# Optimization experiments

Hardware: AMD Instinct MI355X
Metric: run time of the kernel (lower is better)

Reference implementation:

```python
import jax, jax.numpy as jnp
import numpy as np
import math

N, N_OBS, D, H, P = 500000, 200000, 32, 128, 4


def setup_inputs() -> dict:
    key = jax.random.key(0)
    ks = jax.random.split(key, 10)
    h = jax.random.normal(ks[0], (N, H), dtype=jnp.float32)
    p = jax.random.normal(ks[1], (N, 2 * D), dtype=jnp.float32)
    X_obs = jax.random.normal(ks[2], (N_OBS, D), dtype=jnp.float32)
    M_obs = (jax.random.uniform(ks[3], (N_OBS, D)) > 0.5).astype(jnp.float32)
    # unique sorted indices into [0, N) so the scatter-update is well defined
    i_obs = jnp.sort(jax.random.permutation(ks[4], N)[:N_OBS]).astype(jnp.int32)
    std = math.sqrt(2.0 / (4 + P))
    w_prep = std * jax.random.normal(ks[5], (D, 4, P), dtype=jnp.float32)
    bias_prep = 0.1 + jnp.zeros((D, P), dtype=jnp.float32)
    k = 1.0 / math.sqrt(H)
    W_ih = jax.random.uniform(ks[6], (3 * H, P * D), minval=-k, maxval=k, dtype=jnp.float32)
    W_hh = jax.random.uniform(ks[7], (3 * H, H), minval=-k, maxval=k, dtype=jnp.float32)
    b_ih = jax.random.uniform(ks[8], (3 * H,), minval=-k, maxval=k, dtype=jnp.float32)
    b_hh = jax.random.uniform(ks[9], (3 * H,), minval=-k, maxval=k, dtype=jnp.float32)
    return {"h": h, "p": p, "X_obs": X_obs, "M_obs": M_obs, "i_obs": i_obs,
            "w_prep": w_prep, "bias_prep": bias_prep,
            "W_ih": W_ih, "W_hh": W_hh, "b_ih": b_ih, "b_hh": b_hh}


def gru_cell(x, h, W_ih, W_hh, b_ih, b_hh):
    # torch.nn.GRUCell semantics; gate order r, z, n
    gi = x @ W_ih.T + b_ih            # [n, 3H]
    gh = h @ W_hh.T + b_hh            # [n, 3H]
    i_r, i_z, i_n = jnp.split(gi, 3, axis=1)
    h_r, h_z, h_n = jnp.split(gh, 3, axis=1)
    r = jax.nn.sigmoid(i_r + h_r)
    z = jax.nn.sigmoid(i_z + h_z)
    n = jnp.tanh(i_n + r * h_n)
    return (1.0 - z) * n + z * h


def reference(h, p, X_obs, M_obs, i_obs, w_prep, bias_prep, W_ih, W_hh, b_ih, b_hh):
    p_obs = p[i_obs]                                     # gather [n_obs, 2D]
    mean, logvar = jnp.split(p_obs, 2, axis=1)
    lv = jnp.clip(logvar, -10.0, 10.0)
    sigma = jnp.clip(jnp.exp(0.5 * lv), 1e-6, 1e6)
    error = jnp.clip((X_obs - mean) / sigma, -1e6, 1e6)
    log_lik_c = float(np.log(np.sqrt(2 * np.pi)))
    losses = 0.5 * ((error ** 2 + lv + 2.0 * log_lik_c) * M_obs)  # [n_obs, D]
    feats = jnp.stack([X_obs, mean, lv, error], axis=2)  # [n_obs, D, 4]
    gi = jnp.einsum('ndk,dkp->ndp', feats, w_prep) + bias_prep  # per-channel small matmul
    gi = jax.nn.relu(gi) * M_obs[..., None]              # mask broadcast over prep_hidden
    gru_in = gi.reshape(gi.shape[0], D * P)              # [n_obs, D*P], D-major like torch view
    h_obs = h[i_obs]
    h_new = gru_cell(gru_in, h_obs, W_ih, W_hh, b_ih, b_hh)
    h = h.at[i_obs].set(h_new)                           # scatter update
    return (h, losses)
```

## Files before the change

### kernel.cpp

```cpp
#include <hip/hip_runtime.h>


typedef __attribute__((ext_vector_type(8))) short bf16x8;
typedef __attribute__((ext_vector_type(4))) float f32x4;

__device__ inline unsigned short f2bf_rne(float x) {
    union { float f; unsigned int u; } v; v.f = x;
    unsigned int r = (v.u + 0x7fffu + ((v.u >> 16) & 1u)) >> 16;
    return (unsigned short)r;
}
__device__ inline unsigned short f2bf_tr(float x) {
    return (unsigned short)(__float_as_uint(x) >> 16);
}
__device__ inline float bf2f(unsigned short u) {
    return __uint_as_float(((unsigned int)u) << 16);
}
__device__ inline float fast_sigmoid(float x) {
    return __builtin_amdgcn_rcpf(1.f + __expf(-x));
}
__device__ inline float fast_tanh(float x) {
    const float a = fabsf(x);
    const float t = __expf(-2.f * a);
    const float r = (1.f - t) * __builtin_amdgcn_rcpf(1.f + t);
    return __builtin_copysignf(r, x);
}
__device__ inline void gl_lds16(const float* g, float* lds_base) {
    __builtin_amdgcn_global_load_lds(
        (const __attribute__((address_space(1))) void*)g,
        (__attribute__((address_space(3))) void*)lds_base, 16, 0, 0);
}

__global__ __launch_bounds__(256) void k_prepack(const float* __restrict__ W_ih,
                                                 const float* __restrict__ W_hh,
                                                 unsigned short* __restrict__ B) {
    const int i = blockIdx.x * 256 + threadIdx.x;
    const int w    = i / 12288;
    const int rem  = i - w * 12288;
    const int f    = rem >> 9;
    const int rem2 = rem & 511;
    const int l    = rem2 >> 3;
    const int j    = rem2 & 7;
    const int c    = w * 16 + (l & 15);
    const int ko   = (l >> 4) * 8 + j;
    float val;
    if (f < 8) {
        const int k = f * 32 + ko;
        val = (k < 128) ? W_ih[c * 128 + k] : W_hh[c * 128 + (k - 128)];
    } else if (f < 16) {
        const int k = (f - 8) * 32 + ko;
        val = (k < 128) ? W_ih[(128 + c) * 128 + k] : W_hh[(128 + c) * 128 + (k - 128)];
    } else if (f < 20) {
        const int k = (f - 16) * 32 + ko;
        val = W_ih[(256 + c) * 128 + k];
    } else {
        const int k = (f - 20 + 4) * 32 + ko;
        val = W_hh[(256 + c) * 128 + (k - 128)];
    }
    B[i] = f2bf_rne(val);
}

__global__ __launch_bounds__(256) void k_flag(const int* __restrict__ i_obs,
                                              unsigned char* __restrict__ flags, int n) {
    const int i = blockIdx.x * 256 + threadIdx.x;
    if (i < n) flags[i_obs[i]] = 1;
}

__global__ __launch_bounds__(256) void k_copy(const f32x4* __restrict__ src,
                                              f32x4* __restrict__ dst, long n4) {
    long i = (long)blockIdx.x * blockDim.x + threadIdx.x;
    long stride = (long)gridDim.x * blockDim.x;
    for (; i < n4; i += stride) dst[i] = src[i];
}

struct PrefRegs {
    float mean[4], lv[4], X[4], M[4];
    f32x4 hv[4];
    int idx[4];
};

__global__ __launch_bounds__(512) void k_pers(
    const float* __restrict__ h, const float* __restrict__ p,
    const float* __restrict__ X_obs, const float* __restrict__ M_obs,
    const int* __restrict__ i_obs,
    const float* __restrict__ w_prep, const float* __restrict__ bias_prep,
    const unsigned short* __restrict__ Bpk,
    const float* __restrict__ b_ih, const float* __restrict__ b_hh,
    float* __restrict__ out_h, float* __restrict__ out_losses,
    const unsigned char* __restrict__ flags,
    int NT, int chunk, int Nh, int do_copy)
{
    __shared__ unsigned short sA[4 * 8 * 64 * 8];
    __shared__ float hcopy[160 * 128];
    __shared__ int sIdx[64];

    const int tid  = threadIdx.x;
    const int d    = tid & 31;
    const int wid  = tid >> 6;
    const int lane = tid & 63;
    const int cw   = wid * 16 + (lane & 15);

    float wp[16], bp[4];
    #pragma unroll
    for (int t = 0; t < 16; ++t) wp[t] = w_prep[d * 16 + t];
    #pragma unroll
    for (int t = 0; t < 4; ++t) bp[t] = bias_prep[d * 4 + t];

    bf16x8 breg[24];
    {
        const bf16x8* bsrc = reinterpret_cast<const bf16x8*>(Bpk) + wid * 1536;
        #pragma unroll
        for (int f = 0; f < 24; ++f) breg[f] = bsrc[f * 64 + lane];
    }
    const float bR  = b_ih[cw]       + b_hh[cw];
    const float bZ  = b_ih[128 + cw] + b_hh[128 + cw];
    const float bIN = b_ih[256 + cw];
    const float bHN = b_hh[256 + cw];

    const int ksA  = d >> 3;
    const int l16  = ((d >> 1) & 3) * 16;
    const int j0   = (d & 1) * 4;
    const int ksE  = 4 + (cw >> 5);
    const int l16E = ((cw >> 3) & 3) * 16;
    const int jE   = cw & 7;

    const bf16x8* aptr = reinterpret_cast<const bf16x8*>(sA);

    PrefRegs R;

    auto G_load = [&](int t) {
        const int row0 = t * 64;
        #pragma unroll
        for (int ps = 0; ps < 4; ++ps) {
            const int r   = ps * 16 + (tid >> 5);
            const int idx = i_obs[row0 + r];
            R.idx[ps]  = idx;
            R.mean[ps] = p[(size_t)idx * 64 + d];
            R.lv[ps]   = p[(size_t)idx * 64 + 32 + d];
            R.X[ps]    = X_obs[(size_t)(row0 + r) * 32 + d];
            R.M[ps]    = M_obs[(size_t)(row0 + r) * 32 + d];
            R.hv[ps]   = *reinterpret_cast<const f32x4*>(h + (size_t)idx * 128 + d * 4);
        }
    };

    auto COPY_issue = [&](int t) {
        const long rlo = (long)t * chunk;
        const float* hs = h + rlo * 128;
        const int rbase = wid * 20;
        #pragma unroll
        for (int q = 0; q < 10; ++q) {
            const int row = rbase + q * 2;
            gl_lds16(hs + (size_t)row * 128 + lane * 4, &hcopy[row * 128]);
        }
    };

    auto COPY_store = [&](int t) {
        const long rlo = (long)t * chunk;
        f32x4* hd = reinterpret_cast<f32x4*>(out_h + rlo * 128);
        const unsigned char* fl = flags + rlo;
        const f32x4* hc = reinterpret_cast<const f32x4*>(hcopy);
        #pragma unroll
        for (int ii = 0; ii < 10; ++ii) {
            const int i5 = ii * 512 + tid;
            if (!fl[i5 >> 5]) __builtin_nontemporal_store(hc[i5], &hd[i5]);
        }
    };

    auto C_phase = [&](int t) {
        const int row0 = t * 64;
        #pragma unroll
        for (int ps = 0; ps < 4; ++ps) {
            const int r  = ps * 16 + (tid >> 5);
            const int mt = r >> 4;
            if (d == 0) sIdx[r] = R.idx[ps];
            const float lv      = fminf(fmaxf(R.lv[ps], -10.f), 10.f);
            const float inv_sig = __expf(-0.5f * lv);
            const float X = R.X[ps], Mv = R.M[ps], mean = R.mean[ps];
            const float err = fminf(fmaxf((X - mean) * inv_sig, -1e6f), 1e6f);
            out_losses[(size_t)(row0 + r) * 32 + d] =
                0.5f * ((err * err + lv + 1.8378770664093453f) * Mv);
            ushort4 u;
            float g0 = fmaf(X, wp[0], fmaf(mean, wp[4], fmaf(lv, wp[8],  fmaf(err, wp[12], bp[0]))));
            float g1 = fmaf(X, wp[1], fmaf(mean, wp[5], fmaf(lv, wp[9],  fmaf(err, wp[13], bp[1]))));
            float g2 = fmaf(X, wp[2], fmaf(mean, wp[6], fmaf(lv, wp[10], fmaf(err, wp[14], bp[2]))));
            float g3 = fmaf(X, wp[3], fmaf(mean, wp[7], fmaf(lv, wp[11], fmaf(err, wp[15], bp[3]))));
            u.x = f2bf_tr(fmaxf(g0, 0.f) * Mv);
            u.y = f2bf_tr(fmaxf(g1, 0.f) * Mv);
            u.z = f2bf_tr(fmaxf(g2, 0.f) * Mv);
            u.w = f2bf_tr(fmaxf(g3, 0.f) * Mv);
            *reinterpret_cast<ushort4*>(&sA[((mt * 8 + ksA) * 64 + (r & 15) + l16) * 8 + j0]) = u;
            const f32x4 v = R.hv[ps];
            ushort4 uh;
            uh.x = f2bf_tr(v.x); uh.y = f2bf_tr(v.y); uh.z = f2bf_tr(v.z); uh.w = f2bf_tr(v.w);
            *reinterpret_cast<ushort4*>(&sA[((mt * 8 + ksA + 4) * 64 + (r & 15) + l16) * 8 + j0]) = uh;
        }
    };

    auto M_phase = [&]() {
        #pragma unroll
        for (int mt = 0; mt < 4; ++mt) {
            f32x4 accR = {0.f, 0.f, 0.f, 0.f};
            f32x4 accZ = {0.f, 0.f, 0.f, 0.f};
            f32x4 accIN = {0.f, 0.f, 0.f, 0.f};
            f32x4 accHN = {0.f, 0.f, 0.f, 0.f};
            #pragma unroll
            for (int ks = 0; ks < 8; ++ks) {
                const bf16x8 af = aptr[(mt * 8 + ks) * 64 + lane];
                accR = __builtin_amdgcn_mfma_f32_16x16x32_bf16(af, breg[ks],     accR, 0, 0, 0);
                accZ = __builtin_amdgcn_mfma_f32_16x16x32_bf16(af, breg[8 + ks], accZ, 0, 0, 0);
                if (ks < 4) accIN = __builtin_amdgcn_mfma_f32_16x16x32_bf16(af, breg[16 + ks], accIN, 0, 0, 0);
                else        accHN = __builtin_amdgcn_mfma_f32_16x16x32_bf16(af, breg[16 + ks], accHN, 0, 0, 0);
            }
            const int r15b = (lane >> 4) * 4;
            #pragma unroll
            for (int reg = 0; reg < 4; ++reg) {
                const int r15 = r15b + reg;
                const int idx = sIdx[mt * 16 + r15];
                const float hp = bf2f(sA[((mt * 8 + ksE) * 64 + r15 + l16E) * 8 + jE]);
                const float xr  = accR[reg]  + bR;
                const float xz  = accZ[reg]  + bZ;
                const float xin = accIN[reg] + bIN;
                const float xhn = accHN[reg] + bHN;
                const float rg = fast_sigmoid(xr);
                const float zg = fast_sigmoid(xz);
                const float ng = fast_tanh(fmaf(rg, xhn, xin));
                out_h[(size_t)idx * 128 + cw] = fmaf(zg, hp - ng, ng);
            }
        }
    };

    int t = blockIdx.x;
    if (t >= NT) return;
    const int stride = gridDim.x;

    G_load(t);
    C_phase(t);
    __syncthreads();

    for (;;) {
        const int tn = t + stride;
        const bool has_next = (tn < NT);
        if (has_next) G_load(tn);
        if (do_copy) COPY_issue(t);
        M_phase();
        __syncthreads();
        if (do_copy) COPY_store(t);
        if (!has_next) break;
        C_phase(tn);
        __syncthreads();
        t = tn;
    }
}

extern "C" void kernel_launch(void* const* d_in, const int* in_sizes, int n_in,
                              void* d_out, int out_size, void* d_ws, size_t ws_size,
                              hipStream_t stream) {
    const float* h         = (const float*)d_in[0];
    const float* p         = (const float*)d_in[1];
    const float* X_obs     = (const float*)d_in[2];
    const float* M_obs     = (const float*)d_in[3];
    const int*   i_obs     = (const int*)d_in[4];
    const float* w_prep    = (const float*)d_in[5];
    const float* bias_prep = (const float*)d_in[6];
    const float* W_ih      = (const float*)d_in[7];
    const float* W_hh      = (const float*)d_in[8];
    const float* b_ih      = (const float*)d_in[9];
    const float* b_hh      = (const float*)d_in[10];

    const int Nh   = in_sizes[0] / 128;
    const int NOBS = in_sizes[4];
    const int NT   = NOBS / 64;
    const long n4  = (long)Nh * 128 / 4;

    float* out_h      = (float*)d_out;
    float* out_losses = out_h + (size_t)Nh * 128;

    unsigned short* Bpk   = (unsigned short*)d_ws;
    unsigned char*  flags = (unsigned char*)d_ws + (256 << 10);
    const size_t ws_needed = (256 << 10) + (size_t)Nh;

    hipLaunchKernelGGL(k_prepack, dim3(98304 / 256), dim3(256), 0, stream,
                       W_ih, W_hh, Bpk);

    const int chunk = (NT > 0) ? Nh / NT : 0;
    const int GRID  = 512;

    if (ws_size >= ws_needed && chunk == 160 && chunk * NT == Nh && NT * 64 == NOBS) {
        (void)hipMemsetAsync(flags, 0, (size_t)Nh, stream);
        hipLaunchKernelGGL(k_flag, dim3((NOBS + 255) / 256), dim3(256), 0, stream,
                           i_obs, flags, NOBS);
        hipLaunchKernelGGL(k_pers, dim3(GRID), dim3(512), 0, stream,
                           h, p, X_obs, M_obs, i_obs, w_prep, bias_prep, Bpk,
                           b_ih, b_hh, out_h, out_losses, flags, NT, chunk, Nh, 1);
    } else {
        hipLaunchKernelGGL(k_copy, dim3(4096), dim3(256), 0, stream,
                           (const f32x4*)h, (f32x4*)out_h, n4);
        hipLaunchKernelGGL(k_pers, dim3(GRID), dim3(512), 0, stream,
                           h, p, X_obs, M_obs, i_obs, w_prep, bias_prep, Bpk,
                           b_ih, b_hh, out_h, out_losses,
                           (const unsigned char*)nullptr, NT, chunk, Nh, 0);
    }
}
```

Measured before the change: 172.8 us.

## Split h-copy staging into two halves overlapped with M and C phases

Halves the LDS staging buffer for the bulk h copy from 160 rows to 80 rows. The copy is now done in two halves per tile: one half is issued before the M phase and stored after it, and the other is issued before the C phase and stored in the next iteration. The goal is to free LDS, which may allow more blocks per CU, and to spread the copy traffic across both compute phases. The cost is a more complex cross-iteration schedule and an extra tail store, and it relies on the barriers ordering LDS reuse correctly.

```diff
diff --git a/kernel.cpp b/kernel.cpp
--- a/kernel.cpp
+++ b/kernel.cpp
@@ -90,7 +90,7 @@
     int NT, int chunk, int Nh, int do_copy)
 {
     __shared__ unsigned short sA[4 * 8 * 64 * 8];
-    __shared__ float hcopy[160 * 128];
+    __shared__ float buf[80 * 128];
     __shared__ int sIdx[64];
 
     const int tid  = threadIdx.x;
@@ -142,26 +142,29 @@
         }
     };
 
-    auto COPY_issue = [&](int t) {
-        const long rlo = (long)t * chunk;
+    auto COPY_issue_half = [&](int t, int half) {
+        const long rlo = (long)t * chunk + half * 80;
         const float* hs = h + rlo * 128;
-        const int rbase = wid * 20;
-        #pragma unroll
-        for (int q = 0; q < 10; ++q) {
+        const int rbase = wid * 10;
+        #pragma unroll
+        for (int q = 0; q < 5; ++q) {
             const int row = rbase + q * 2;
-            gl_lds16(hs + (size_t)row * 128 + lane * 4, &hcopy[row * 128]);
-        }
-    };
-
-    auto COPY_store = [&](int t) {
-        const long rlo = (long)t * chunk;
+            gl_lds16(hs + (size_t)row * 128 + lane * 4, &buf[row * 128]);
+        }
+    };
+
+    auto COPY_store_half = [&](int t, int half) {
+        const long rlo = (long)t * chunk + half * 80;
         f32x4* hd = reinterpret_cast<f32x4*>(out_h + rlo * 128);
         const unsigned char* fl = flags + rlo;
-        const f32x4* hc = reinterpret_cast<const f32x4*>(hcopy);
-        #pragma unroll
-        for (int ii = 0; ii < 10; ++ii) {
-            const int i5 = ii * 512 + tid;
-            if (!fl[i5 >> 5]) __builtin_nontemporal_store(hc[i5], &hd[i5]);
+        const f32x4* b4 = reinterpret_cast<const f32x4*>(buf);
+        const int rbase = wid * 10;
+        #pragma unroll
+        for (int q = 0; q < 5; ++q) {
+            const int row = rbase + q * 2 + (lane >> 5);
+            const int c4  = lane & 31;
+            const f32x4 v = b4[row * 32 + c4];
+            if (!fl[row]) __builtin_nontemporal_store(v, &hd[row * 32 + c4]);
         }
     };
 
@@ -236,17 +239,29 @@
     C_phase(t);
     __syncthreads();
 
+    int tprev = -1;
+
     for (;;) {
         const int tn = t + stride;
         const bool has_next = (tn < NT);
         if (has_next) G_load(tn);
-        if (do_copy) COPY_issue(t);
+        if (do_copy) {
+            if (tprev >= 0) COPY_store_half(tprev, 1);
+            COPY_issue_half(t, 0);
+        }
         M_phase();
         __syncthreads();
-        if (do_copy) COPY_store(t);
-        if (!has_next) break;
-        C_phase(tn);
+        if (do_copy) {
+            COPY_store_half(t, 0);
+            COPY_issue_half(t, 1);
+        }
+        if (has_next) C_phase(tn);
         __syncthreads();
+        if (!has_next) {
+            if (do_copy) COPY_store_half(t, 1);
+            break;
+        }
+        tprev = t;
         t = tn;
     }
 }
```

Result: slower. 181.1 us (+4.8%).
